# Optimization experiments

Measured on AMD Instinct MI355X. Metric: run time of the kernel, lower is better.

## Reference

```python
import jax, jax.numpy as jnp
import numpy as np

N, C, H, W = 8, 16, 512, 512
GRID = 8                     # 8x8 grid of 64x64 blocks => components
K = GRID * GRID + 1          # label 0 = background, 1..64 = components


def setup_inputs() -> dict:
    key = jax.random.key(0)
    k1, k2 = jax.random.split(key)
    color = jax.random.normal(k1, (N, C, H, W), dtype=jnp.float32)
    # blocky ground-truth probability map so connected components == blocks
    bh = H // GRID
    block_vals = jax.random.uniform(k2, (N, GRID, GRID), dtype=jnp.float32)
    gt = jnp.repeat(jnp.repeat(block_vals, bh, axis=1), bh, axis=2)[:, None, :, :]
    # per-pixel component label: block id (1..64) where gt>0.5, else 0
    block_ids = (jnp.arange(GRID)[:, None] * GRID + jnp.arange(GRID)[None, :] + 1).astype(jnp.int32)
    block_ids_full = jnp.repeat(jnp.repeat(block_ids, bh, axis=0), bh, axis=1)
    block_ids_full = jnp.broadcast_to(block_ids_full[None], (N, H, W))
    labels = jnp.where(gt[:, 0] > 0.5, block_ids_full, 0)
    return {"color": color, "gt": gt, "labels": labels}


def reference(color, gt, labels):
    lambda_inter, margin, thr, min_pixels, eps = 0.4, 0.5, 0.5, 20.0, 1e-6
    Nb, Cc, Hh, Ww = color.shape
    Kc = K
    sub = (gt[:, 0] > thr).astype(color.dtype)      # (N,H,W)
    bg = 1.0 - sub
    bg_cnt = bg.sum(axis=(1, 2))                    # (N,)
    # background masked mean per image: (N,C)
    m_bg = jnp.einsum('nchw,nhw->nc', color, bg) / (bg_cnt + eps)[:, None]
    # per-component segment reductions (single pass over pixels)
    feat = color.transpose(0, 2, 3, 1).reshape(-1, Cc)          # (N*H*W, C)
    seg = (labels + jnp.arange(Nb, dtype=labels.dtype)[:, None, None] * Kc).reshape(-1)
    counts = jax.ops.segment_sum(jnp.ones(seg.shape[0], color.dtype), seg, Nb * Kc).reshape(Nb, Kc)
    fsum = jax.ops.segment_sum(feat, seg, Nb * Kc).reshape(Nb, Kc, Cc)
    sqsum = jax.ops.segment_sum((feat * feat).sum(-1), seg, Nb * Kc).reshape(Nb, Kc)
    denom = counts + eps
    m_sub = fsum / denom[..., None]                 # (N,K,C)
    # intra: sum_{p in comp} ||f_p - m_sub||^2 / (count+eps), expanded form
    intra = (sqsum - 2.0 * (m_sub * fsum).sum(-1) + counts * (m_sub * m_sub).sum(-1)) / denom
    dist = jnp.sqrt(((m_sub - m_bg[:, None, :]) ** 2).sum(-1) + 1e-12)
    inter = jnp.maximum(margin - dist, 0.0) ** 2
    valid = (counts >= min_pixels) & (jnp.arange(Kc)[None, :] > 0) & (bg_cnt[:, None] >= min_pixels)
    v = valid.astype(color.dtype)
    total = v.sum()
    safe_total = jnp.maximum(total, 1.0)
    intra_avg = (intra * v).sum() / safe_total
    inter_avg = (inter * v).sum() / safe_total
    loss = jnp.where(total > 0, intra_avg + lambda_inter * inter_avg, 0.0)
    return loss
```

## Files before the change

### kernel.cpp

```cpp
#include <hip/hip_runtime.h>


namespace {
constexpr int NIMG = 8;
constexpr int NCH  = 16;
constexpr int HWPX = 512 * 512;
constexpr int KSEG = 65;
constexpr int NF   = 18;
constexpr float EPSV   = 1e-6f;
constexpr float MARGIN = 0.5f;
constexpr float LAMBDA = 0.4f;
constexpr float MINPIX = 20.0f;
}

__global__ __launch_bounds__(256) void accum_kernel(
    const float* __restrict__ color,
    const int*   __restrict__ labels,
    float* __restrict__ ws)
{
    __shared__ float tab[KSEG * NF];
    const int tid = threadIdx.x;
    for (int i = tid; i < KSEG * NF; i += 256) tab[i] = 0.0f;
    __syncthreads();

    const int n = blockIdx.y;
    const float* colN = color  + (size_t)n * NCH * HWPX;
    const int*   labN = labels + (size_t)n * HWPX;

    const int grp  = tid >> 4;
    const int l16  = tid & 15;
    const int wgrp = (tid & 63) >> 4;

    const int stride = gridDim.x * 1024;
    for (int base = blockIdx.x * 1024; base < HWPX; base += stride) {
        const int p = base + grp * 64 + l16 * 4;
        const int4 lab = *reinterpret_cast<const int4*>(labN + p);
        const int  lab0 = __shfl(lab.x, 0, 16);
        const bool uni_t = (lab.x == lab.y) && (lab.x == lab.z) &&
                           (lab.x == lab.w) && (lab.x == lab0);
        const unsigned long long b = __ballot((int)uni_t);
        const unsigned long long m = 0xFFFFull << (wgrp * 16);

        if ((b & m) == m) {
            float fs[NCH];
            float sq = 0.0f;
            #pragma unroll
            for (int c = 0; c < NCH; ++c) {
                const float4 v = *reinterpret_cast<const float4*>(
                    colN + (size_t)c * HWPX + p);
                fs[c] = (v.x + v.y) + (v.z + v.w);
                sq += v.x * v.x + v.y * v.y + v.z * v.z + v.w * v.w;
            }
            #pragma unroll
            for (int c = 0; c < 8; ++c) {
                const float snd = (l16 & 8) ? fs[c] : fs[c + 8];
                const float kp  = (l16 & 8) ? fs[c + 8] : fs[c];
                fs[c] = kp + __shfl_xor(snd, 8, 16);
            }
            #pragma unroll
            for (int c = 0; c < 4; ++c) {
                const float snd = (l16 & 4) ? fs[c] : fs[c + 4];
                const float kp  = (l16 & 4) ? fs[c + 4] : fs[c];
                fs[c] = kp + __shfl_xor(snd, 4, 16);
            }
            #pragma unroll
            for (int c = 0; c < 2; ++c) {
                const float snd = (l16 & 2) ? fs[c] : fs[c + 2];
                const float kp  = (l16 & 2) ? fs[c + 2] : fs[c];
                fs[c] = kp + __shfl_xor(snd, 2, 16);
            }
            {
                const float snd = (l16 & 1) ? fs[0] : fs[1];
                const float kp  = (l16 & 1) ? fs[1] : fs[0];
                fs[0] = kp + __shfl_xor(snd, 1, 16);
            }
            sq += __shfl_xor(sq, 8, 16);
            sq += __shfl_xor(sq, 4, 16);
            sq += __shfl_xor(sq, 2, 16);
            sq += __shfl_xor(sq, 1, 16);

            float* seg = tab + lab0 * NF;
            atomicAdd(seg + 2 + l16, fs[0]);
            if (l16 == 0) {
                atomicAdd(seg + 0, 64.0f);
                atomicAdd(seg + 1, sq);
            }
        } else {
            const int labv[4] = {lab.x, lab.y, lab.z, lab.w};
            for (int i = 0; i < 4; ++i) {
                float sqp = 0.0f;
                float* seg = tab + labv[i] * NF;
                for (int c = 0; c < NCH; ++c) {
                    const float x = colN[(size_t)c * HWPX + p + i];
                    sqp += x * x;
                    atomicAdd(seg + 2 + c, x);
                }
                atomicAdd(seg + 0, 1.0f);
                atomicAdd(seg + 1, sqp);
            }
        }
    }

    __syncthreads();
    float* wsN = ws + (size_t)n * KSEG * NF;
    for (int i = tid; i < KSEG * NF; i += 256) {
        const float v = tab[i];
        if (v != 0.0f) atomicAdd(wsN + i, v);
    }
}

__global__ __launch_bounds__(256) void finalize_kernel(
    const float* __restrict__ ws, float* __restrict__ out)
{
    __shared__ float mbg[NIMG][NCH];
    __shared__ float bgcnt[NIMG];
    __shared__ float r0[256], r1[256], r2[256];
    const int tid = threadIdx.x;
    if (tid < NIMG * NCH) {
        const int n = tid / NCH, c = tid % NCH;
        const float* b = ws + (size_t)n * KSEG * NF;
        const float cnt = b[0];
        mbg[n][c] = b[2 + c] / (cnt + EPSV);
        if (c == 0) bgcnt[n] = cnt;
    }
    __syncthreads();

    float vsum = 0.0f, intraS = 0.0f, interS = 0.0f;
    for (int idx = tid; idx < NIMG * KSEG; idx += 256) {
        const int n = idx / KSEG, k = idx % KSEG;
        if (k == 0) continue;
        const float* s = ws + ((size_t)n * KSEG + k) * NF;
        const float cnt = s[0], sq = s[1];
        const float denom = cnt + EPSV;
        float d2 = 0.0f, msf = 0.0f, msm = 0.0f;
        #pragma unroll
        for (int c = 0; c < NCH; ++c) {
            const float f  = s[2 + c];
            const float mu = f / denom;
            msf += mu * f;
            msm += mu * mu;
            const float dd = mu - mbg[n][c];
            d2 += dd * dd;
        }
        const float intra = (sq - 2.0f * msf + cnt * msm) / denom;
        const float dist  = sqrtf(d2 + 1e-12f);
        const float t     = fmaxf(MARGIN - dist, 0.0f);
        const float inter = t * t;
        if ((cnt >= MINPIX) && (bgcnt[n] >= MINPIX)) {
            vsum += 1.0f; intraS += intra; interS += inter;
        }
    }
    r0[tid] = vsum; r1[tid] = intraS; r2[tid] = interS;
    __syncthreads();
    for (int sft = 128; sft; sft >>= 1) {
        if (tid < sft) {
            r0[tid] += r0[tid + sft];
            r1[tid] += r1[tid + sft];
            r2[tid] += r2[tid + sft];
        }
        __syncthreads();
    }
    if (tid == 0) {
        const float total = r0[0];
        const float safe  = fmaxf(total, 1.0f);
        out[0] = (total > 0.0f) ? (r1[0] + LAMBDA * r2[0]) / safe : 0.0f;
    }
}

extern "C" void kernel_launch(void* const* d_in, const int* in_sizes, int n_in,
                              void* d_out, int out_size, void* d_ws, size_t ws_size,
                              hipStream_t stream) {
    const float* color  = (const float*)d_in[0];
    const int*   labels = (const int*)d_in[2];
    float* ws  = (float*)d_ws;
    float* out = (float*)d_out;

    hipMemsetAsync(ws, 0, (size_t)NIMG * KSEG * NF * sizeof(float), stream);

    dim3 grid(128, NIMG);
    accum_kernel<<<grid, 256, 0, stream>>>(color, labels, ws);
    finalize_kernel<<<1, 256, 0, stream>>>(ws, out);
}
```

Before: 36.82 us.

## Fuse finalize into accumulation via last-block ticket and issue all loads upfront

Removes the separate finalize kernel launch: each block bumps a global ticket after flushing its partial table, and the last block computes the loss. The grid doubles to 256 blocks per image so each thread handles exactly one tile, which lets all 16 channel float4 loads be issued before the branch. The non-uniform path reuses the registers instead of reloading from memory. Writing the output through a device pointer stashed by a tiny extra kernel still costs a launch, and holding 64 floats per thread in registers may reduce occupancy.

```diff
diff --git a/kernel.cpp b/kernel.cpp
--- a/kernel.cpp
+++ b/kernel.cpp
@@ -7,6 +7,8 @@
 constexpr int HWPX = 512 * 512;
 constexpr int KSEG = 65;
 constexpr int NF   = 18;
+constexpr int TABF = NIMG * KSEG * NF;
+constexpr int NBLK = 256;
 constexpr float EPSV   = 1e-6f;
 constexpr float MARGIN = 0.5f;
 constexpr float LAMBDA = 0.4f;
@@ -19,6 +21,7 @@
     float* __restrict__ ws)
 {
     __shared__ float tab[KSEG * NF];
+    __shared__ int   s_last;
     const int tid = threadIdx.x;
     for (int i = tid; i < KSEG * NF; i += 256) tab[i] = 0.0f;
     __syncthreads();
@@ -31,106 +34,117 @@
     const int l16  = tid & 15;
     const int wgrp = (tid & 63) >> 4;
 
-    const int stride = gridDim.x * 1024;
-    for (int base = blockIdx.x * 1024; base < HWPX; base += stride) {
-        const int p = base + grp * 64 + l16 * 4;
-        const int4 lab = *reinterpret_cast<const int4*>(labN + p);
-        const int  lab0 = __shfl(lab.x, 0, 16);
-        const bool uni_t = (lab.x == lab.y) && (lab.x == lab.z) &&
-                           (lab.x == lab.w) && (lab.x == lab0);
-        const unsigned long long b = __ballot((int)uni_t);
-        const unsigned long long m = 0xFFFFull << (wgrp * 16);
-
-        if ((b & m) == m) {
-            float fs[NCH];
-            float sq = 0.0f;
+    const int p = blockIdx.x * 1024 + grp * 64 + l16 * 4;
+
+    const int4 lab = *reinterpret_cast<const int4*>(labN + p);
+    float4 v[NCH];
+    #pragma unroll
+    for (int c = 0; c < NCH; ++c)
+        v[c] = *reinterpret_cast<const float4*>(colN + (size_t)c * HWPX + p);
+
+    const int  lab0 = __shfl(lab.x, 0, 16);
+    const bool uni_t = (lab.x == lab.y) && (lab.x == lab.z) &&
+                       (lab.x == lab.w) && (lab.x == lab0);
+    const unsigned long long b = __ballot((int)uni_t);
+    const unsigned long long m = 0xFFFFull << (wgrp * 16);
+
+    if ((b & m) == m) {
+        float fs[NCH];
+        float sq = 0.0f;
+        #pragma unroll
+        for (int c = 0; c < NCH; ++c) {
+            fs[c] = (v[c].x + v[c].y) + (v[c].z + v[c].w);
+            sq += v[c].x * v[c].x + v[c].y * v[c].y
+                + v[c].z * v[c].z + v[c].w * v[c].w;
+        }
+        #pragma unroll
+        for (int c = 0; c < 8; ++c) {
+            const float snd = (l16 & 8) ? fs[c] : fs[c + 8];
+            const float kp  = (l16 & 8) ? fs[c + 8] : fs[c];
+            fs[c] = kp + __shfl_xor(snd, 8, 16);
+        }
+        #pragma unroll
+        for (int c = 0; c < 4; ++c) {
+            const float snd = (l16 & 4) ? fs[c] : fs[c + 4];
+            const float kp  = (l16 & 4) ? fs[c + 4] : fs[c];
+            fs[c] = kp + __shfl_xor(snd, 4, 16);
+        }
+        #pragma unroll
+        for (int c = 0; c < 2; ++c) {
+            const float snd = (l16 & 2) ? fs[c] : fs[c + 2];
+            const float kp  = (l16 & 2) ? fs[c + 2] : fs[c];
+            fs[c] = kp + __shfl_xor(snd, 2, 16);
+        }
+        {
+            const float snd = (l16 & 1) ? fs[0] : fs[1];
+            const float kp  = (l16 & 1) ? fs[1] : fs[0];
+            fs[0] = kp + __shfl_xor(snd, 1, 16);
+        }
+        sq += __shfl_xor(sq, 8, 16);
+        sq += __shfl_xor(sq, 4, 16);
+        sq += __shfl_xor(sq, 2, 16);
+        sq += __shfl_xor(sq, 1, 16);
+
+        float* seg = tab + lab0 * NF;
+        atomicAdd(seg + 2 + l16, fs[0]);
+        if (l16 == 0) {
+            atomicAdd(seg + 0, 64.0f);
+            atomicAdd(seg + 1, sq);
+        }
+    } else {
+        const int labv[4] = {lab.x, lab.y, lab.z, lab.w};
+        #pragma unroll
+        for (int i = 0; i < 4; ++i) {
+            float sqp = 0.0f;
+            float* seg = tab + labv[i] * NF;
             #pragma unroll
             for (int c = 0; c < NCH; ++c) {
-                const float4 v = *reinterpret_cast<const float4*>(
-                    colN + (size_t)c * HWPX + p);
-                fs[c] = (v.x + v.y) + (v.z + v.w);
-                sq += v.x * v.x + v.y * v.y + v.z * v.z + v.w * v.w;
+                const float x = (i == 0) ? v[c].x : (i == 1) ? v[c].y
+                              : (i == 2) ? v[c].z : v[c].w;
+                sqp += x * x;
+                atomicAdd(seg + 2 + c, x);
             }
-            #pragma unroll
-            for (int c = 0; c < 8; ++c) {
-                const float snd = (l16 & 8) ? fs[c] : fs[c + 8];
-                const float kp  = (l16 & 8) ? fs[c + 8] : fs[c];
-                fs[c] = kp + __shfl_xor(snd, 8, 16);
-            }
-            #pragma unroll
-            for (int c = 0; c < 4; ++c) {
-                const float snd = (l16 & 4) ? fs[c] : fs[c + 4];
-                const float kp  = (l16 & 4) ? fs[c + 4] : fs[c];
-                fs[c] = kp + __shfl_xor(snd, 4, 16);
-            }
-            #pragma unroll
-            for (int c = 0; c < 2; ++c) {
-                const float snd = (l16 & 2) ? fs[c] : fs[c + 2];
-                const float kp  = (l16 & 2) ? fs[c + 2] : fs[c];
-                fs[c] = kp + __shfl_xor(snd, 2, 16);
-            }
-            {
-                const float snd = (l16 & 1) ? fs[0] : fs[1];
-                const float kp  = (l16 & 1) ? fs[1] : fs[0];
-                fs[0] = kp + __shfl_xor(snd, 1, 16);
-            }
-            sq += __shfl_xor(sq, 8, 16);
-            sq += __shfl_xor(sq, 4, 16);
-            sq += __shfl_xor(sq, 2, 16);
-            sq += __shfl_xor(sq, 1, 16);
-
-            float* seg = tab + lab0 * NF;
-            atomicAdd(seg + 2 + l16, fs[0]);
-            if (l16 == 0) {
-                atomicAdd(seg + 0, 64.0f);
-                atomicAdd(seg + 1, sq);
-            }
-        } else {
-            const int labv[4] = {lab.x, lab.y, lab.z, lab.w};
-            for (int i = 0; i < 4; ++i) {
-                float sqp = 0.0f;
-                float* seg = tab + labv[i] * NF;
-                for (int c = 0; c < NCH; ++c) {
-                    const float x = colN[(size_t)c * HWPX + p + i];
-                    sqp += x * x;
-                    atomicAdd(seg + 2 + c, x);
-                }
-                atomicAdd(seg + 0, 1.0f);
-                atomicAdd(seg + 1, sqp);
-            }
+            atomicAdd(seg + 0, 1.0f);
+            atomicAdd(seg + 1, sqp);
         }
     }
 
     __syncthreads();
     float* wsN = ws + (size_t)n * KSEG * NF;
     for (int i = tid; i < KSEG * NF; i += 256) {
-        const float v = tab[i];
-        if (v != 0.0f) atomicAdd(wsN + i, v);
-    }
-}
-
-__global__ __launch_bounds__(256) void finalize_kernel(
-    const float* __restrict__ ws, float* __restrict__ out)
-{
+        const float x = tab[i];
+        if (x != 0.0f) atomicAdd(wsN + i, x);
+    }
+    __syncthreads();
+
+    if (tid == 0) {
+        __threadfence();
+        unsigned* ticket = reinterpret_cast<unsigned*>(ws + TABF);
+        const unsigned old = atomicAdd(ticket, 1u);
+        s_last = (old == (unsigned)(NBLK * NIMG - 1));
+    }
+    __syncthreads();
+    if (!s_last) return;
+    __threadfence();
+
     __shared__ float mbg[NIMG][NCH];
     __shared__ float bgcnt[NIMG];
     __shared__ float r0[256], r1[256], r2[256];
-    const int tid = threadIdx.x;
     if (tid < NIMG * NCH) {
-        const int n = tid / NCH, c = tid % NCH;
-        const float* b = ws + (size_t)n * KSEG * NF;
-        const float cnt = b[0];
-        mbg[n][c] = b[2 + c] / (cnt + EPSV);
-        if (c == 0) bgcnt[n] = cnt;
+        const int ni = tid / NCH, c = tid % NCH;
+        const float* bp = ws + (size_t)ni * KSEG * NF;
+        const float cnt = bp[0];
+        mbg[ni][c] = bp[2 + c] / (cnt + EPSV);
+        if (c == 0) bgcnt[ni] = cnt;
     }
     __syncthreads();
 
     float vsum = 0.0f, intraS = 0.0f, interS = 0.0f;
     for (int idx = tid; idx < NIMG * KSEG; idx += 256) {
-        const int n = idx / KSEG, k = idx % KSEG;
+        const int ni = idx / KSEG, k = idx % KSEG;
         if (k == 0) continue;
-        const float* s = ws + ((size_t)n * KSEG + k) * NF;
-        const float cnt = s[0], sq = s[1];
+        const float* s = ws + ((size_t)ni * KSEG + k) * NF;
+        const float cnt = s[0], sq2 = s[1];
         const float denom = cnt + EPSV;
         float d2 = 0.0f, msf = 0.0f, msm = 0.0f;
         #pragma unroll
@@ -139,14 +153,14 @@
             const float mu = f / denom;
             msf += mu * f;
             msm += mu * mu;
-            const float dd = mu - mbg[n][c];
+            const float dd = mu - mbg[ni][c];
             d2 += dd * dd;
         }
-        const float intra = (sq - 2.0f * msf + cnt * msm) / denom;
+        const float intra = (sq2 - 2.0f * msf + cnt * msm) / denom;
         const float dist  = sqrtf(d2 + 1e-12f);
         const float t     = fmaxf(MARGIN - dist, 0.0f);
         const float inter = t * t;
-        if ((cnt >= MINPIX) && (bgcnt[n] >= MINPIX)) {
+        if ((cnt >= MINPIX) && (bgcnt[ni] >= MINPIX)) {
             vsum += 1.0f; intraS += intra; interS += inter;
         }
     }
@@ -161,10 +175,18 @@
         __syncthreads();
     }
     if (tid == 0) {
+        float* out = reinterpret_cast<float*>(
+            reinterpret_cast<uintptr_t>(ws + TABF + 2));
+        float** outp = reinterpret_cast<float**>(out);
         const float total = r0[0];
         const float safe  = fmaxf(total, 1.0f);
-        out[0] = (total > 0.0f) ? (r1[0] + LAMBDA * r2[0]) / safe : 0.0f;
-    }
+        (*outp)[0] = (total > 0.0f) ? (r1[0] + LAMBDA * r2[0]) / safe : 0.0f;
+    }
+}
+
+__global__ void stash_outptr(float* ws, float* out) {
+    if (threadIdx.x == 0)
+        *reinterpret_cast<float**>(ws + TABF + 2) = out;
 }
 
 extern "C" void kernel_launch(void* const* d_in, const int* in_sizes, int n_in,
@@ -175,9 +197,9 @@
     float* ws  = (float*)d_ws;
     float* out = (float*)d_out;
 
-    hipMemsetAsync(ws, 0, (size_t)NIMG * KSEG * NF * sizeof(float), stream);
-
-    dim3 grid(128, NIMG);
+    hipMemsetAsync(ws, 0, (size_t)(TABF + 2) * sizeof(float), stream);
+    stash_outptr<<<1, 64, 0, stream>>>(ws, out);
+
+    dim3 grid(NBLK, NIMG);
     accum_kernel<<<grid, 256, 0, stream>>>(color, labels, ws);
-    finalize_kernel<<<1, 256, 0, stream>>>(ws, out);
-}
+}
```

New measurement: 102.9 us. +179.6%, slower.

## Precompute per-span uniform labels in a separate kernel, replacing memset

Applied to the files above, without the earlier changes.

Adds a pre-pass kernel that reads the label map once and writes one compact entry per 64-pixel span: the span's label if uniform, otherwise -1. The same kernel zeroes the global accumulation table, which replaces the memset call. The accumulation kernel then reads one int per span instead of a full int4 label vector plus shuffle and ballot, and reloads labels only for mixed spans. The cost is an extra kernel launch and a serial dependency, while the label bytes are still read once in the pre-pass.

```diff
diff --git a/kernel.cpp b/kernel.cpp
--- a/kernel.cpp
+++ b/kernel.cpp
@@ -7,41 +7,68 @@
 constexpr int HWPX = 512 * 512;
 constexpr int KSEG = 65;
 constexpr int NF   = 18;
+constexpr int SPANS = HWPX / 64;
+constexpr int TABF  = NIMG * KSEG * NF;
+constexpr int WS_TAB = NIMG * SPANS;
 constexpr float EPSV   = 1e-6f;
 constexpr float MARGIN = 0.5f;
 constexpr float LAMBDA = 0.4f;
 constexpr float MINPIX = 20.0f;
 }
 
+__global__ __launch_bounds__(256) void spanlab_kernel(
+    const int* __restrict__ labels, int* __restrict__ spanlab,
+    float* __restrict__ tab)
+{
+    const int n   = blockIdx.y;
+    const int tid = threadIdx.x;
+    const int grp = tid >> 4, l16 = tid & 15, wgrp = (tid & 63) >> 4;
+    const int span = blockIdx.x * 16 + grp;
+    const int p    = span * 64 + l16 * 4;
+
+    if (n == 0) {
+        if (tid < 37) {
+            const int idx = blockIdx.x * 37 + tid;
+            if (idx < TABF) tab[idx] = 0.0f;
+        }
+    }
+
+    const int4 lab = *reinterpret_cast<const int4*>(labels + (size_t)n * HWPX + p);
+    const int  lab0 = __shfl(lab.x, 0, 16);
+    const bool uni  = (lab.x == lab.y) && (lab.x == lab.z) &&
+                      (lab.x == lab.w) && (lab.x == lab0);
+    const unsigned long long b = __ballot((int)uni);
+    const unsigned long long m = 0xFFFFull << (wgrp * 16);
+    if (l16 == 0)
+        spanlab[n * SPANS + span] = ((b & m) == m) ? lab0 : -1;
+}
+
 __global__ __launch_bounds__(256) void accum_kernel(
     const float* __restrict__ color,
     const int*   __restrict__ labels,
-    float* __restrict__ ws)
+    const int*   __restrict__ spanlab,
+    float* __restrict__ tab)
 {
-    __shared__ float tab[KSEG * NF];
+    __shared__ float ltab[KSEG * NF];
     const int tid = threadIdx.x;
-    for (int i = tid; i < KSEG * NF; i += 256) tab[i] = 0.0f;
+    for (int i = tid; i < KSEG * NF; i += 256) ltab[i] = 0.0f;
     __syncthreads();
 
     const int n = blockIdx.y;
     const float* colN = color  + (size_t)n * NCH * HWPX;
     const int*   labN = labels + (size_t)n * HWPX;
-
-    const int grp  = tid >> 4;
-    const int l16  = tid & 15;
-    const int wgrp = (tid & 63) >> 4;
+    const int*   slN  = spanlab + n * SPANS;
+
+    const int grp = tid >> 4;
+    const int l16 = tid & 15;
 
     const int stride = gridDim.x * 1024;
     for (int base = blockIdx.x * 1024; base < HWPX; base += stride) {
-        const int p = base + grp * 64 + l16 * 4;
-        const int4 lab = *reinterpret_cast<const int4*>(labN + p);
-        const int  lab0 = __shfl(lab.x, 0, 16);
-        const bool uni_t = (lab.x == lab.y) && (lab.x == lab.z) &&
-                           (lab.x == lab.w) && (lab.x == lab0);
-        const unsigned long long b = __ballot((int)uni_t);
-        const unsigned long long m = 0xFFFFull << (wgrp * 16);
-
-        if ((b & m) == m) {
+        const int span = (base >> 6) + grp;
+        const int p    = base + grp * 64 + l16 * 4;
+        const int slab = slN[span];
+
+        if (slab >= 0) {
             float fs[NCH];
             float sq = 0.0f;
             #pragma unroll
@@ -79,17 +106,18 @@
             sq += __shfl_xor(sq, 2, 16);
             sq += __shfl_xor(sq, 1, 16);
 
-            float* seg = tab + lab0 * NF;
+            float* seg = ltab + slab * NF;
             atomicAdd(seg + 2 + l16, fs[0]);
             if (l16 == 0) {
                 atomicAdd(seg + 0, 64.0f);
                 atomicAdd(seg + 1, sq);
             }
         } else {
-            const int labv[4] = {lab.x, lab.y, lab.z, lab.w};
+            const int4 lb = *reinterpret_cast<const int4*>(labN + p);
+            const int labv[4] = {lb.x, lb.y, lb.z, lb.w};
             for (int i = 0; i < 4; ++i) {
                 float sqp = 0.0f;
-                float* seg = tab + labv[i] * NF;
+                float* seg = ltab + labv[i] * NF;
                 for (int c = 0; c < NCH; ++c) {
                     const float x = colN[(size_t)c * HWPX + p + i];
                     sqp += x * x;
@@ -102,15 +130,15 @@
     }
 
     __syncthreads();
-    float* wsN = ws + (size_t)n * KSEG * NF;
+    float* tabN = tab + (size_t)n * KSEG * NF;
     for (int i = tid; i < KSEG * NF; i += 256) {
-        const float v = tab[i];
-        if (v != 0.0f) atomicAdd(wsN + i, v);
+        const float x = ltab[i];
+        if (x != 0.0f) atomicAdd(tabN + i, x);
     }
 }
 
 __global__ __launch_bounds__(256) void finalize_kernel(
-    const float* __restrict__ ws, float* __restrict__ out)
+    const float* __restrict__ tab, float* __restrict__ out)
 {
     __shared__ float mbg[NIMG][NCH];
     __shared__ float bgcnt[NIMG];
@@ -118,7 +146,7 @@
     const int tid = threadIdx.x;
     if (tid < NIMG * NCH) {
         const int n = tid / NCH, c = tid % NCH;
-        const float* b = ws + (size_t)n * KSEG * NF;
+        const float* b = tab + (size_t)n * KSEG * NF;
         const float cnt = b[0];
         mbg[n][c] = b[2 + c] / (cnt + EPSV);
         if (c == 0) bgcnt[n] = cnt;
@@ -129,7 +157,7 @@
     for (int idx = tid; idx < NIMG * KSEG; idx += 256) {
         const int n = idx / KSEG, k = idx % KSEG;
         if (k == 0) continue;
-        const float* s = ws + ((size_t)n * KSEG + k) * NF;
+        const float* s = tab + ((size_t)n * KSEG + k) * NF;
         const float cnt = s[0], sq = s[1];
         const float denom = cnt + EPSV;
         float d2 = 0.0f, msf = 0.0f, msm = 0.0f;
@@ -175,9 +203,14 @@
     float* ws  = (float*)d_ws;
     float* out = (float*)d_out;
 
-    hipMemsetAsync(ws, 0, (size_t)NIMG * KSEG * NF * sizeof(float), stream);
-
-    dim3 grid(128, NIMG);
-    accum_kernel<<<grid, 256, 0, stream>>>(color, labels, ws);
-    finalize_kernel<<<1, 256, 0, stream>>>(ws, out);
-}
+    int*   spanlab = (int*)ws;
+    float* tab     = ws + WS_TAB;
+
+    dim3 gridA(SPANS / 16, NIMG);
+    spanlab_kernel<<<gridA, 256, 0, stream>>>(labels, spanlab, tab);
+
+    dim3 gridB(128, NIMG);
+    accum_kernel<<<gridB, 256, 0, stream>>>(color, labels, spanlab, tab);
+
+    finalize_kernel<<<1, 256, 0, stream>>>(tab, out);
+}
```

Measured after the change: 35.85 us. 2.6% less time.
